# Kernel tuning notes

Measured on AMD Instinct MI355X. Metric: run time of the kernel, lower is better.

## Reference

```python
import jax, jax.numpy as jnp
import numpy as np

WINDOW = 20  # local attention window, per create_sparse_mask


def _make_mask(rng, n, sparsity_ratio=0.1):
    # local band: |i - j| <= window//2 (covers start/end clamping and the diagonal)
    idx = jnp.arange(n)
    mask = jnp.abs(idx[:, None] - idx[None, :]) <= (WINDOW // 2)
    # random edges: n_random (i, j) pairs set to 1 (duplicates harmless)
    n_random = int(sparsity_ratio * n * n)
    k1, k2 = jax.random.split(rng)
    ri = jax.random.randint(k1, (n_random,), 0, n)
    rj = jax.random.randint(k2, (n_random,), 0, n)
    mask = mask.at[ri, rj].set(True)
    return mask  # [n, n] bool


def setup_inputs() -> dict:
    rng = jax.random.key(0)
    kq, kk, kv, km = jax.random.split(rng, 4)
    B, H, S, D = 1, 8, 4096, 32
    return {
        "query": jax.random.normal(kq, (B, H, S, D), dtype=jnp.float32),
        "key": jax.random.normal(kk, (B, H, S, D), dtype=jnp.float32),
        "value": jax.random.normal(kv, (B, H, S, D), dtype=jnp.float32),
        "mask": _make_mask(km, S, sparsity_ratio=0.1),
    }


def reference(query, key, value, mask):
    # query/key/value: [B, H, S, D]; mask: [S, S] bool (True = attend)
    head_dim = query.shape[-1]
    scale = 1.0 / jnp.sqrt(jnp.float32(head_dim))
    scores = jnp.einsum("bhqd,bhkd->bhqk", query, key) * scale
    # torch: scores = scores * mask; masked_fill(mask == 0, -inf) -> equivalent to where
    scores = jnp.where(mask[None, None, :, :], scores, -jnp.inf)
    attn = jax.nn.softmax(scores, axis=-1)
    attn = jnp.nan_to_num(attn, nan=0.0)
    return jnp.einsum("bhqk,bhkd->bhqd", attn, value)
```

## Files before the change

kernel.cpp:

```cpp
#include <hip/hip_runtime.h>
#include <hip/hip_bf16.h>


#define S_  4096
#define D_  32
#define H_  8

typedef _Float16 half8 __attribute__((ext_vector_type(8)));
typedef __fp16 fp16x2 __attribute__((ext_vector_type(2)));
typedef short short8 __attribute__((ext_vector_type(8)));
typedef short short4v __attribute__((ext_vector_type(4)));
typedef float float4v __attribute__((ext_vector_type(4)));
typedef unsigned short ushort_t;
typedef unsigned int u32;

__device__ inline ushort_t f2h(float x) {
    union { _Float16 h; ushort_t u; } c; c.h = (_Float16)x; return c.u;
}

__global__ __launch_bounds__(256)
void prepass(const float* __restrict__ Q, const float* __restrict__ K,
             const float* __restrict__ V, const int* __restrict__ mask,
             ushort_t* __restrict__ Qh, ushort_t* __restrict__ Kt,
             ushort_t* __restrict__ Vt, ushort_t* __restrict__ mlane)
{
    __shared__ u32 msh[4096];
    const int bx = blockIdx.x;
    const int tid = threadIdx.x;
    union U8 { ushort_t u[8]; short8 v; };

    if (bx < 512) {
        const int e0 = (bx * 256 + tid) * 8;
        const float c = 0.17677669529663687f * 1.4426950408889634f;
        float4 a = *(const float4*)(Q + e0);
        float4 b = *(const float4*)(Q + e0 + 4);
        float f[8] = {a.x*c, a.y*c, a.z*c, a.w*c, b.x*c, b.y*c, b.z*c, b.w*c};
        U8 o;
#pragma unroll
        for (int i = 0; i < 8; ++i) o.u[i] = f2h(f[i]);
        *(short8*)(Qh + e0) = o.v;
    } else if (bx < 1024) {
        const int e0 = ((bx - 512) * 256 + tid) * 8;
        const int n = (e0 >> 3) & 15, quad = (e0 >> 7) & 3, t16 = (e0 >> 9) & 3;
        const int kt = (e0 >> 11) & 63, h = e0 >> 17;
        const int krow = kt * 64 + t16 * 16 + n;
        const float* src = K + ((size_t)h * S_ + krow) * D_ + quad * 8;
        float4 a = *(const float4*)src;
        float4 b = *(const float4*)(src + 4);
        float f[8] = {a.x, a.y, a.z, a.w, b.x, b.y, b.z, b.w};
        U8 o;
#pragma unroll
        for (int i = 0; i < 8; ++i) o.u[i] = f2h(f[i]);
        *(short8*)(Kt + e0) = o.v;
    } else if (bx < 1536) {
        const int e0 = ((bx - 1024) * 256 + tid) * 8;
        const int n = (e0 >> 3) & 15, quad = (e0 >> 7) & 3;
        const int dhalf = (e0 >> 9) & 1, khalf = (e0 >> 10) & 1;
        const int kt = (e0 >> 11) & 63, h = e0 >> 17;
        const int d = dhalf * 16 + n;
        const int pbase = khalf * 32 + quad * 8;
        U8 o;
#pragma unroll
        for (int j = 0; j < 8; ++j) {
            int p = pbase + j;
            int krow = kt * 64 + (p & 3) * 16 + (p >> 2);
            o.u[j] = f2h(V[((size_t)h * S_ + krow) * D_ + d]);
        }
        *(short8*)(Vt + e0) = o.v;
    } else {
        const int mb = bx - 1536;
        const int qt16 = mb >> 2, cc = mb & 3;
#pragma unroll
        for (int i = 0; i < 16; ++i) {
            int4 m4 = *(const int4*)(mask + (size_t)(qt16 * 16 + i) * S_ + cc * 1024 + tid * 4);
            u32 v = (m4.x != 0 ? 1u : 0u) | (m4.y != 0 ? 0x100u : 0u)
                  | (m4.z != 0 ? 0x10000u : 0u) | (m4.w != 0 ? 0x1000000u : 0u);
            msh[i * 256 + tid] = v;
        }
        __syncthreads();
        const int kt_local = tid >> 4, j = tid & 15;
        const int quad = j >> 2, n2 = j & 3;
        u32 o16[4] = {0, 0, 0, 0};
#pragma unroll
        for (int t16 = 0; t16 < 4; ++t16)
#pragma unroll
            for (int reg = 0; reg < 4; ++reg) {
                u32 v = msh[(quad * 4 + reg) * 256 + kt_local * 16 + t16 * 4 + n2];
                const int bp = t16 * 4 + reg;
                o16[0] |= (v & 1u) << bp;
                o16[1] |= ((v >> 8) & 1u) << bp;
                o16[2] |= ((v >> 16) & 1u) << bp;
                o16[3] |= ((v >> 24) & 1u) << bp;
            }
        union { u32 w[2]; short4v s; } pk;
        pk.w[0] = o16[0] | (o16[1] << 16);
        pk.w[1] = o16[2] | (o16[3] << 16);
        const int kt = cc * 16 + kt_local;
        *(short4v*)(mlane + ((size_t)(qt16 * 64 + kt) * 64 + j * 4)) = pk.s;
    }
}


#define PS_STRIDE 72

__device__ inline void gl_lds16(const ushort_t* g, ushort_t* l) {
    __builtin_amdgcn_global_load_lds((const __attribute__((address_space(1))) void*)g,
                                     (__attribute__((address_space(3))) void*)l,
                                     16, 0, 0);
}

__global__ __launch_bounds__(512, 4)
void attn_mfma(const ushort_t* __restrict__ Qh, const ushort_t* __restrict__ Kt,
               const ushort_t* __restrict__ Vt, const ushort_t* __restrict__ mlane,
               float* __restrict__ out)
{
    __shared__ __align__(16) ushort_t sm[8192 + 8 * 16 * PS_STRIDE];
    ushort_t* K_s  = sm;
    ushort_t* Vt_s = sm + 4096;

    const int h  = blockIdx.y;
    const int q0 = blockIdx.x * 64;
    const int tid = threadIdx.x;
    const int w = tid >> 6, l = tid & 63;
    const int half = w >> 2, wl = w & 3;
    const int n16 = l & 15, quad = l >> 4;

    ushort_t* Ps = sm + 8192 + w * 16 * PS_STRIDE;

    const int qt16_u = __builtin_amdgcn_readfirstlane(blockIdx.x * 4 + wl);
    const ushort_t* mlw = mlane + ((size_t)qt16_u << 12);

    const int qrow = q0 + wl * 16 + n16;
    const half8 qh = *(const half8*)(Qh + ((size_t)h * S_ + qrow) * D_ + quad * 8);

    half8 ones;
#pragma unroll
    for (int i = 0; i < 8; ++i) ones[i] = (_Float16)1.0f;

    float4v o0 = {0.f, 0.f, 0.f, 0.f};
    float4v o1 = {0.f, 0.f, 0.f, 0.f};
    float4v lacc = {0.f, 0.f, 0.f, 0.f};

    const int hbase = half * 2048;

    for (int i = 0; i < 32; ++i) {
        const int kt = half * 32 + i;
        __syncthreads();
        const size_t tb = ((size_t)(h * 64 + kt)) * 2048 + wl * 512 + l * 8;
        gl_lds16(Kt + tb, K_s  + hbase + wl * 512);
        gl_lds16(Vt + tb, Vt_s + hbase + wl * 512);

        const u32 ml = mlw[kt * 64 + l];
        __syncthreads();

        float pv[4][4];
#pragma unroll
        for (int t16 = 0; t16 < 4; ++t16) {
            const half8 kb = *(const half8*)(K_s + hbase + (t16 * 4 + quad) * 128 + n16 * 8);
            float4v c = {0.f, 0.f, 0.f, 0.f};
            c = __builtin_amdgcn_mfma_f32_16x16x32_f16(qh, kb, c, 0, 0, 0);
#pragma unroll
            for (int reg = 0; reg < 4; ++reg) {
                float e = exp2f(c[reg]);
                pv[t16][reg] = (ml & (1u << (t16 * 4 + reg))) ? e : 0.f;
            }
        }
#pragma unroll
        for (int reg = 0; reg < 4; ++reg) {
            fp16x2 h01 = __builtin_amdgcn_cvt_pkrtz(pv[0][reg], pv[1][reg]);
            fp16x2 h23 = __builtin_amdgcn_cvt_pkrtz(pv[2][reg], pv[3][reg]);
            union { fp16x2 h[2]; short4v s; } pk;
            pk.h[0] = h01; pk.h[1] = h23;
            *(short4v*)(Ps + (quad * 4 + reg) * PS_STRIDE + n16 * 4) = pk.s;
        }
        asm volatile("" ::: "memory");

#pragma unroll
        for (int khalf = 0; khalf < 2; ++khalf) {
            const half8 pa = *(const half8*)(Ps + n16 * PS_STRIDE + khalf * 32 + quad * 8);
            const half8 v0 = *(const half8*)(Vt_s + hbase + ((khalf * 2 + 0) * 4 + quad) * 128 + n16 * 8);
            const half8 v1 = *(const half8*)(Vt_s + hbase + ((khalf * 2 + 1) * 4 + quad) * 128 + n16 * 8);
            o0 = __builtin_amdgcn_mfma_f32_16x16x32_f16(pa, v0, o0, 0, 0, 0);
            o1 = __builtin_amdgcn_mfma_f32_16x16x32_f16(pa, v1, o1, 0, 0, 0);
            lacc = __builtin_amdgcn_mfma_f32_16x16x32_f16(pa, ones, lacc, 0, 0, 0);
        }
    }

    __syncthreads();
    float* red = (float*)sm;
    const int RSTR = 16 * 33 + 16;
    if (half == 1) {
        float* ro = red + wl * RSTR;
#pragma unroll
        for (int reg = 0; reg < 4; ++reg) {
            const int r = quad * 4 + reg;
            ro[r * 33 + n16]      = o0[reg];
            ro[r * 33 + 16 + n16] = o1[reg];
            if (n16 == 0) ro[16 * 33 + r] = lacc[reg];
        }
    }
    __syncthreads();
    if (half == 0) {
        const float* ro = red + wl * RSTR;
#pragma unroll
        for (int reg = 0; reg < 4; ++reg) {
            const int r = quad * 4 + reg;
            const float inv = 1.0f / (lacc[reg] + ro[16 * 33 + r]);
            const int row = q0 + wl * 16 + r;
            float* orow = out + ((size_t)h * S_ + row) * D_;
            orow[n16]      = (o0[reg] + ro[r * 33 + n16]) * inv;
            orow[16 + n16] = (o1[reg] + ro[r * 33 + 16 + n16]) * inv;
        }
    }
}


#define QT 64
#define KT 64
#define NSUB 4
#define KPT 16

__global__ __launch_bounds__(256, 2)
void sparse_attn_fp32(const float* __restrict__ Q, const float* __restrict__ K,
                      const float* __restrict__ V, const int* __restrict__ mask,
                      float* __restrict__ out)
{
    __shared__ float Ks[KT][D_];
    __shared__ float Vs[KT][D_];
    __shared__ float red_o[NSUB][QT][D_ + 1];
    __shared__ float red_l[NSUB][QT];

    const int h = blockIdx.y;
    const int q0 = blockIdx.x * QT;
    const int tid = threadIdx.x;
    const int ql = tid & 63;
    const int sub = tid >> 6;
    const int q = q0 + ql;
    const float scale = 0.17677669529663687f;

    float4 qreg[8];
    const float4* qrow = (const float4*)(Q + ((size_t)h * S_ + q) * D_);
#pragma unroll
    for (int i = 0; i < 8; ++i) qreg[i] = qrow[i];

    float o[D_];
#pragma unroll
    for (int d = 0; d < D_; ++d) o[d] = 0.f;
    float lsum0 = 0.f;

    const float* Kh = K + (size_t)h * S_ * D_;
    const float* Vh = V + (size_t)h * S_ * D_;

    for (int jt = 0; jt < S_; jt += KT) {
        __syncthreads();
        {
            const float4* gK = (const float4*)(Kh + (size_t)jt * D_);
            const float4* gV = (const float4*)(Vh + (size_t)jt * D_);
            float4* sK = (float4*)&Ks[0][0];
            float4* sV = (float4*)&Vs[0][0];
            sK[tid] = gK[tid]; sK[tid + 256] = gK[tid + 256];
            sV[tid] = gV[tid]; sV[tid + 256] = gV[tid + 256];
        }
        __syncthreads();

        int4 m4[4];
        {
            const int4* mr = (const int4*)(mask + (size_t)q * S_ + jt + sub * KPT);
#pragma unroll
            for (int i = 0; i < 4; ++i) m4[i] = mr[i];
        }
        const int* mb = (const int*)m4;

#pragma unroll
        for (int kk = 0; kk < KPT; ++kk) {
            const int jl = sub * KPT + kk;
            const float4* krow = (const float4*)&Ks[jl][0];
            float s = 0.f;
#pragma unroll
            for (int i = 0; i < 8; ++i) {
                float4 kv = krow[i];
                s += qreg[i].x * kv.x + qreg[i].y * kv.y + qreg[i].z * kv.z + qreg[i].w * kv.w;
            }
            const float p = mb[kk] ? __expf(s * scale) : 0.f;
            lsum0 += p;
            const float4* vrow = (const float4*)&Vs[jl][0];
#pragma unroll
            for (int i = 0; i < 8; ++i) {
                float4 vv = vrow[i];
                o[i * 4 + 0] += p * vv.x;
                o[i * 4 + 1] += p * vv.y;
                o[i * 4 + 2] += p * vv.z;
                o[i * 4 + 3] += p * vv.w;
            }
        }
    }

#pragma unroll
    for (int d = 0; d < D_; ++d) red_o[sub][ql][d] = o[d];
    red_l[sub][ql] = lsum0;
    __syncthreads();

    const int eq = tid & 63;
    const int dg = tid >> 6;
    float acc[8];
#pragma unroll
    for (int i = 0; i < 8; ++i) acc[i] = 0.f;
    float lsum = 0.f;
#pragma unroll
    for (int s2 = 0; s2 < NSUB; ++s2) {
        lsum += red_l[s2][eq];
#pragma unroll
        for (int i = 0; i < 8; ++i) acc[i] += red_o[s2][eq][dg * 8 + i];
    }
    const float inv = 1.0f / lsum;
    float* orow = out + ((size_t)h * S_ + q0 + eq) * D_ + dg * 8;
#pragma unroll
    for (int i = 0; i < 8; ++i) orow[i] = acc[i] * inv;
}


extern "C" void kernel_launch(void* const* d_in, const int* in_sizes, int n_in,
                              void* d_out, int out_size, void* d_ws, size_t ws_size,
                              hipStream_t stream) {
    const float* Q = (const float*)d_in[0];
    const float* K = (const float*)d_in[1];
    const float* V = (const float*)d_in[2];
    const int* mask = (const int*)d_in[3];
    float* out = (float*)d_out;

    const size_t MB = 1024 * 1024;
    if (ws_size < 8 * MB) {
        dim3 grid(S_ / QT, H_);
        sparse_attn_fp32<<<grid, 256, 0, stream>>>(Q, K, V, mask, out);
        return;
    }

    char* ws = (char*)d_ws;
    ushort_t* Qh = (ushort_t*)(ws + 0 * MB);
    ushort_t* Kt = (ushort_t*)(ws + 2 * MB);
    ushort_t* Vt = (ushort_t*)(ws + 4 * MB);
    ushort_t* mlane = (ushort_t*)(ws + 6 * MB);

    prepass<<<2560, 256, 0, stream>>>(Q, K, V, mask, Qh, Kt, Vt, mlane);

    dim3 grid(S_ / 64, H_);
    attn_mfma<<<grid, 512, 0, stream>>>(Qh, Kt, Vt, mlane, out);
}
```

Before: 163.0 us.

## Double-buffer K/V tiles in LDS, split prepass, use native exp2

The attention kernel now double-buffers K and V tiles in shared memory. The next tile's global-to-LDS load is issued before computing on the current one, which cuts the loop to one barrier per iteration instead of two. The prepass is split into separate QKV-conversion and mask-packing kernels, and exp2f is replaced by the hardware exp2 builtin when available. Shared memory roughly doubles and launch bounds drop to 2 blocks per CU, which may reduce occupancy. The extra kernel launch adds a little overhead.

```diff
diff --git a/kernel.cpp b/kernel.cpp
--- a/kernel.cpp
+++ b/kernel.cpp
@@ -14,17 +14,22 @@
 typedef unsigned short ushort_t;
 typedef unsigned int u32;
 
+#if __has_builtin(__builtin_amdgcn_exp2f)
+#define EXP2(x) __builtin_amdgcn_exp2f(x)
+#else
+#define EXP2(x) exp2f(x)
+#endif
+
 __device__ inline ushort_t f2h(float x) {
     union { _Float16 h; ushort_t u; } c; c.h = (_Float16)x; return c.u;
 }
 
 __global__ __launch_bounds__(256)
-void prepass(const float* __restrict__ Q, const float* __restrict__ K,
-             const float* __restrict__ V, const int* __restrict__ mask,
-             ushort_t* __restrict__ Qh, ushort_t* __restrict__ Kt,
-             ushort_t* __restrict__ Vt, ushort_t* __restrict__ mlane)
+void prep_qkv(const float* __restrict__ Q, const float* __restrict__ K,
+              const float* __restrict__ V,
+              ushort_t* __restrict__ Qh, ushort_t* __restrict__ Kt,
+              ushort_t* __restrict__ Vt)
 {
-    __shared__ u32 msh[4096];
     const int bx = blockIdx.x;
     const int tid = threadIdx.x;
     union U8 { ushort_t u[8]; short8 v; };
@@ -52,7 +57,7 @@
 #pragma unroll
         for (int i = 0; i < 8; ++i) o.u[i] = f2h(f[i]);
         *(short8*)(Kt + e0) = o.v;
-    } else if (bx < 1536) {
+    } else {
         const int e0 = ((bx - 1024) * 256 + tid) * 8;
         const int n = (e0 >> 3) & 15, quad = (e0 >> 7) & 3;
         const int dhalf = (e0 >> 9) & 1, khalf = (e0 >> 10) & 1;
@@ -67,37 +72,43 @@
             o.u[j] = f2h(V[((size_t)h * S_ + krow) * D_ + d]);
         }
         *(short8*)(Vt + e0) = o.v;
-    } else {
-        const int mb = bx - 1536;
-        const int qt16 = mb >> 2, cc = mb & 3;
-#pragma unroll
-        for (int i = 0; i < 16; ++i) {
-            int4 m4 = *(const int4*)(mask + (size_t)(qt16 * 16 + i) * S_ + cc * 1024 + tid * 4);
-            u32 v = (m4.x != 0 ? 1u : 0u) | (m4.y != 0 ? 0x100u : 0u)
-                  | (m4.z != 0 ? 0x10000u : 0u) | (m4.w != 0 ? 0x1000000u : 0u);
-            msh[i * 256 + tid] = v;
-        }
-        __syncthreads();
-        const int kt_local = tid >> 4, j = tid & 15;
-        const int quad = j >> 2, n2 = j & 3;
-        u32 o16[4] = {0, 0, 0, 0};
-#pragma unroll
-        for (int t16 = 0; t16 < 4; ++t16)
-#pragma unroll
-            for (int reg = 0; reg < 4; ++reg) {
-                u32 v = msh[(quad * 4 + reg) * 256 + kt_local * 16 + t16 * 4 + n2];
-                const int bp = t16 * 4 + reg;
-                o16[0] |= (v & 1u) << bp;
-                o16[1] |= ((v >> 8) & 1u) << bp;
-                o16[2] |= ((v >> 16) & 1u) << bp;
-                o16[3] |= ((v >> 24) & 1u) << bp;
-            }
-        union { u32 w[2]; short4v s; } pk;
-        pk.w[0] = o16[0] | (o16[1] << 16);
-        pk.w[1] = o16[2] | (o16[3] << 16);
-        const int kt = cc * 16 + kt_local;
-        *(short4v*)(mlane + ((size_t)(qt16 * 64 + kt) * 64 + j * 4)) = pk.s;
-    }
+    }
+}
+
+__global__ __launch_bounds__(256)
+void prep_mask(const int* __restrict__ mask, ushort_t* __restrict__ mlane)
+{
+    __shared__ u32 msh[4096];
+    const int tid = threadIdx.x;
+    const int mb = blockIdx.x;
+    const int qt16 = mb >> 2, cc = mb & 3;
+#pragma unroll
+    for (int i = 0; i < 16; ++i) {
+        int4 m4 = *(const int4*)(mask + (size_t)(qt16 * 16 + i) * S_ + cc * 1024 + tid * 4);
+        u32 v = (m4.x != 0 ? 1u : 0u) | (m4.y != 0 ? 0x100u : 0u)
+              | (m4.z != 0 ? 0x10000u : 0u) | (m4.w != 0 ? 0x1000000u : 0u);
+        msh[i * 256 + tid] = v;
+    }
+    __syncthreads();
+    const int kt_local = tid >> 4, j = tid & 15;
+    const int quad = j >> 2, n2 = j & 3;
+    u32 o16[4] = {0, 0, 0, 0};
+#pragma unroll
+    for (int t16 = 0; t16 < 4; ++t16)
+#pragma unroll
+        for (int reg = 0; reg < 4; ++reg) {
+            u32 v = msh[(quad * 4 + reg) * 256 + kt_local * 16 + t16 * 4 + n2];
+            const int bp = t16 * 4 + reg;
+            o16[0] |= (v & 1u) << bp;
+            o16[1] |= ((v >> 8) & 1u) << bp;
+            o16[2] |= ((v >> 16) & 1u) << bp;
+            o16[3] |= ((v >> 24) & 1u) << bp;
+        }
+    union { u32 w[2]; short4v s; } pk;
+    pk.w[0] = o16[0] | (o16[1] << 16);
+    pk.w[1] = o16[2] | (o16[3] << 16);
+    const int kt = cc * 16 + kt_local;
+    *(short4v*)(mlane + ((size_t)(qt16 * 64 + kt) * 64 + j * 4)) = pk.s;
 }
 
 
@@ -109,14 +120,14 @@
                                      16, 0, 0);
 }
 
-__global__ __launch_bounds__(512, 4)
+__global__ __launch_bounds__(512, 2)
 void attn_mfma(const ushort_t* __restrict__ Qh, const ushort_t* __restrict__ Kt,
                const ushort_t* __restrict__ Vt, const ushort_t* __restrict__ mlane,
                float* __restrict__ out)
 {
-    __shared__ __align__(16) ushort_t sm[8192 + 8 * 16 * PS_STRIDE];
+    __shared__ __align__(16) ushort_t sm[16384 + 8 * 16 * PS_STRIDE];
     ushort_t* K_s  = sm;
-    ushort_t* Vt_s = sm + 4096;
+    ushort_t* Vt_s = sm + 8192;
 
     const int h  = blockIdx.y;
     const int q0 = blockIdx.x * 64;
@@ -125,7 +136,7 @@
     const int half = w >> 2, wl = w & 3;
     const int n16 = l & 15, quad = l >> 4;
 
-    ushort_t* Ps = sm + 8192 + w * 16 * PS_STRIDE;
+    ushort_t* Ps = sm + 16384 + w * 16 * PS_STRIDE;
 
     const int qt16_u = __builtin_amdgcn_readfirstlane(blockIdx.x * 4 + wl);
     const ushort_t* mlw = mlane + ((size_t)qt16_u << 12);
@@ -141,27 +152,37 @@
     float4v o1 = {0.f, 0.f, 0.f, 0.f};
     float4v lacc = {0.f, 0.f, 0.f, 0.f};
 
-    const int hbase = half * 2048;
+    const int hb = half * 4096;
+    const int kt_base = half * 32;
+
+    {
+        const size_t tb = ((size_t)(h * 64 + kt_base)) * 2048 + wl * 512 + l * 8;
+        gl_lds16(Kt + tb, K_s  + hb + wl * 512);
+        gl_lds16(Vt + tb, Vt_s + hb + wl * 512);
+    }
+    __syncthreads();
 
     for (int i = 0; i < 32; ++i) {
-        const int kt = half * 32 + i;
-        __syncthreads();
-        const size_t tb = ((size_t)(h * 64 + kt)) * 2048 + wl * 512 + l * 8;
-        gl_lds16(Kt + tb, K_s  + hbase + wl * 512);
-        gl_lds16(Vt + tb, Vt_s + hbase + wl * 512);
+        const int kt = kt_base + i;
+        const int cb = hb + (i & 1) * 2048;
+        if (i < 31) {
+            const int nb = hb + ((i + 1) & 1) * 2048;
+            const size_t tb = ((size_t)(h * 64 + kt + 1)) * 2048 + wl * 512 + l * 8;
+            gl_lds16(Kt + tb, K_s  + nb + wl * 512);
+            gl_lds16(Vt + tb, Vt_s + nb + wl * 512);
+        }
 
         const u32 ml = mlw[kt * 64 + l];
-        __syncthreads();
 
         float pv[4][4];
 #pragma unroll
         for (int t16 = 0; t16 < 4; ++t16) {
-            const half8 kb = *(const half8*)(K_s + hbase + (t16 * 4 + quad) * 128 + n16 * 8);
+            const half8 kb = *(const half8*)(K_s + cb + (t16 * 4 + quad) * 128 + n16 * 8);
             float4v c = {0.f, 0.f, 0.f, 0.f};
             c = __builtin_amdgcn_mfma_f32_16x16x32_f16(qh, kb, c, 0, 0, 0);
 #pragma unroll
             for (int reg = 0; reg < 4; ++reg) {
-                float e = exp2f(c[reg]);
+                float e = EXP2(c[reg]);
                 pv[t16][reg] = (ml & (1u << (t16 * 4 + reg))) ? e : 0.f;
             }
         }
@@ -169,8 +190,8 @@
         for (int reg = 0; reg < 4; ++reg) {
             fp16x2 h01 = __builtin_amdgcn_cvt_pkrtz(pv[0][reg], pv[1][reg]);
             fp16x2 h23 = __builtin_amdgcn_cvt_pkrtz(pv[2][reg], pv[3][reg]);
-            union { fp16x2 h[2]; short4v s; } pk;
-            pk.h[0] = h01; pk.h[1] = h23;
+            union { fp16x2 hh[2]; short4v s; } pk;
+            pk.hh[0] = h01; pk.hh[1] = h23;
             *(short4v*)(Ps + (quad * 4 + reg) * PS_STRIDE + n16 * 4) = pk.s;
         }
         asm volatile("" ::: "memory");
@@ -178,15 +199,16 @@
 #pragma unroll
         for (int khalf = 0; khalf < 2; ++khalf) {
             const half8 pa = *(const half8*)(Ps + n16 * PS_STRIDE + khalf * 32 + quad * 8);
-            const half8 v0 = *(const half8*)(Vt_s + hbase + ((khalf * 2 + 0) * 4 + quad) * 128 + n16 * 8);
-            const half8 v1 = *(const half8*)(Vt_s + hbase + ((khalf * 2 + 1) * 4 + quad) * 128 + n16 * 8);
+            const half8 v0 = *(const half8*)(Vt_s + cb + ((khalf * 2 + 0) * 4 + quad) * 128 + n16 * 8);
+            const half8 v1 = *(const half8*)(Vt_s + cb + ((khalf * 2 + 1) * 4 + quad) * 128 + n16 * 8);
             o0 = __builtin_amdgcn_mfma_f32_16x16x32_f16(pa, v0, o0, 0, 0, 0);
             o1 = __builtin_amdgcn_mfma_f32_16x16x32_f16(pa, v1, o1, 0, 0, 0);
             lacc = __builtin_amdgcn_mfma_f32_16x16x32_f16(pa, ones, lacc, 0, 0, 0);
         }
-    }
-
-    __syncthreads();
+
+        __syncthreads();
+    }
+
     float* red = (float*)sm;
     const int RSTR = 16 * 33 + 16;
     if (half == 1) {
@@ -341,7 +363,8 @@
     ushort_t* Vt = (ushort_t*)(ws + 4 * MB);
     ushort_t* mlane = (ushort_t*)(ws + 6 * MB);
 
-    prepass<<<2560, 256, 0, stream>>>(Q, K, V, mask, Qh, Kt, Vt, mlane);
+    prep_qkv<<<1536, 256, 0, stream>>>(Q, K, V, Qh, Kt, Vt);
+    prep_mask<<<1024, 256, 0, stream>>>(mask, mlane);
 
     dim3 grid(S_ / 64, H_);
     attn_mfma<<<grid, 512, 0, stream>>>(Qh, Kt, Vt, mlane, out);
```

Result: faster. 143.1 us, median of 2 (-12.2%).
